# Kernel tuning notes

Measured on AMD Instinct MI355X. Metric: run time of the kernel, lower is better.

Reference implementation:

```python
import jax, jax.numpy as jnp
import numpy as np

N = 20000
E = 320000
IN_DIM = 256
HID = 128
OUT = 64
HEADS = [4, 1]
NEG_SLOPE = 0.2


def setup_inputs() -> dict:
    key = jax.random.key(0)
    ks = jax.random.split(key, 12)
    x = jax.random.normal(ks[0], (N, IN_DIM), dtype=jnp.float32)
    src = jax.random.randint(ks[1], (E,), 0, N, dtype=jnp.int32)
    dst = jax.random.randint(ks[2], (E,), 0, N, dtype=jnp.int32)
    # Layer 0: in=256 -> heads=4, feat=128
    H0, D0 = HEADS[0], HID
    W1 = jax.random.normal(ks[3], (IN_DIM, H0 * D0), dtype=jnp.float32) * (1.0 / np.sqrt(IN_DIM))
    al1 = jax.random.normal(ks[4], (H0, D0), dtype=jnp.float32) * 0.1
    ar1 = jax.random.normal(ks[5], (H0, D0), dtype=jnp.float32) * 0.1
    b1 = jnp.zeros((H0 * D0,), dtype=jnp.float32)
    # Layer 1: in=4*128=512 -> heads=1, feat=64
    IN2 = H0 * D0
    H1, D1 = HEADS[1], OUT
    W2 = jax.random.normal(ks[6], (IN2, H1 * D1), dtype=jnp.float32) * (1.0 / np.sqrt(IN2))
    al2 = jax.random.normal(ks[7], (H1, D1), dtype=jnp.float32) * 0.1
    ar2 = jax.random.normal(ks[8], (H1, D1), dtype=jnp.float32) * 0.1
    b2 = jnp.zeros((H1 * D1,), dtype=jnp.float32)
    return {"x": x, "src": src, "dst": dst, "W1": W1, "al1": al1, "ar1": ar1, "b1": b1,
            "W2": W2, "al2": al2, "ar2": ar2, "b2": b2}


def gat_conv(h, src, dst, W, al, ar, b, num_heads, out_feats):
    # h: [N, F_in]; DGL GATConv, eval mode (no dropout), allow_zero_in_degree.
    feat = (h @ W).reshape(-1, num_heads, out_feats)          # [N,H,D]
    el = jnp.sum(feat * al, axis=-1)                          # [N,H]
    er = jnp.sum(feat * ar, axis=-1)                          # [N,H]
    e = jax.nn.leaky_relu(el[src] + er[dst], NEG_SLOPE)       # [E,H]
    # edge softmax over incoming edges of each dst node (numerically stable)
    m = jax.ops.segment_max(e, dst, num_segments=N)           # [N,H] (-inf for 0-in-degree)
    ex = jnp.exp(e - m[dst])                                  # [E,H]
    s = jax.ops.segment_sum(ex, dst, num_segments=N)          # [N,H]
    alpha = ex / s[dst]                                       # [E,H]
    msg = feat[src] * alpha[:, :, None]                       # [E,H,D]
    rst = jax.ops.segment_sum(msg, dst, num_segments=N)       # [N,H,D]
    return rst + b.reshape(1, num_heads, out_feats)


def reference(x, src, dst, W1, al1, ar1, b1, W2, al2, ar2, b2):
    h = gat_conv(x, src, dst, W1, al1, ar1, b1, HEADS[0], HID)   # [N,4,128]
    h = jax.nn.elu(h)                                            # activation on non-last layer
    h = h.reshape(N, HEADS[0] * HID)                             # flatten(1)
    h = gat_conv(h, src, dst, W2, al2, ar2, b2, HEADS[1], OUT)   # [N,1,64]
    return h.mean(axis=1)                                        # [N,64]
```

## Files before the change

kernel.cpp:

```cpp
#include <hip/hip_runtime.h>
#include <hip/hip_bf16.h>
#include <cstdint>
#include <cstddef>

#define N_NODES 20000
#define N_EDGES 320000
#define IN_DIM  256
#define HID     128
#define OUT_DIM 64
#define H0      4
#define CAP     64

static __device__ __forceinline__ float leaky(float x) { return x > 0.f ? x : 0.2f * x; }

using short8  = __attribute__((ext_vector_type(8))) short;
using short4v = __attribute__((ext_vector_type(4))) short;
using f32x4   = __attribute__((ext_vector_type(4))) float;

struct HL { short h; short l; };
static __device__ __forceinline__ HL split_bf16(float x) {
  HL r;
  __hip_bfloat16 hb = __float2bfloat16(x);
  float hf = __bfloat162float(hb);
  __hip_bfloat16 lb = __float2bfloat16(x - hf);
  r.h = *(short*)&hb;
  r.l = *(short*)&lb;
  return r;
}

static __device__ __forceinline__ short f2bf_bits(float x) {
  __hip_bfloat16 hb = __float2bfloat16(x);
  return *(short*)&hb;
}

static __device__ __forceinline__ float bf16bits_to_f32(short b) {
  uint32_t u = ((uint32_t)(uint16_t)b) << 16;
  return __uint_as_float(u);
}

static __device__ __forceinline__ void fma8(float a, short8 f, float* acc) {
  const uint32_t* d = (const uint32_t*)&f;
#pragma unroll
  for (int q = 0; q < 4; q++) {
    uint32_t u = d[q];
    float lo = __uint_as_float(u << 16);
    float hi = __uint_as_float(u & 0xFFFF0000u);
    acc[2 * q]     += a * lo;
    acc[2 * q + 1] += a * hi;
  }
}

__global__ void presplit_all_kernel(const float* __restrict__ x,
                                    const float* __restrict__ W1,
                                    const float* __restrict__ W2,
                                    short* __restrict__ xh,
                                    short* __restrict__ w1h, short* __restrict__ w1l,
                                    short* __restrict__ w2h, short* __restrict__ w2l,
                                    int* __restrict__ fill) {
  const int X4  = N_NODES * IN_DIM / 4;
  const int NW1 = IN_DIM * (H0 * HID);
  const int NW2 = (H0 * HID) * OUT_DIM;
  int i = blockIdx.x * 256 + threadIdx.x;
  if (i < X4) {
    int base = i * 4;
    float4 v = *(const float4*)&x[base];
    short4v hv;
    hv[0] = f2bf_bits(v.x); hv[1] = f2bf_bits(v.y);
    hv[2] = f2bf_bits(v.z); hv[3] = f2bf_bits(v.w);
    *(short4v*)&xh[base] = hv;
    return;
  }
  int j = i - X4;
  if (j < NW1) {
    int nn = j / IN_DIM, kk = j - nn * IN_DIM;
    HL e = split_bf16(W1[(size_t)kk * (H0 * HID) + nn]);
    w1h[j] = e.h; w1l[j] = e.l;
    return;
  }
  int k = j - NW1;
  if (k < NW2) {
    int nn = k / (H0 * HID), kk = k - nn * (H0 * HID);
    HL e = split_bf16(W2[(size_t)kk * OUT_DIM + nn]);
    w2h[k] = e.h; w2l[k] = e.l;
    return;
  }
  int z = k - NW2;
  if (z < N_NODES) fill[z] = 0;
}

#define LDK 40

template <int BM, int BN, int NH>
static __device__ void gemm_body(int h, int row0,
                                 const short* __restrict__ A,
                                 const short* __restrict__ Bth,
                                 const short* __restrict__ Btl,
                                 float* __restrict__ C,
                                 __hip_bfloat16* __restrict__ Cb,
                                 const float* __restrict__ alv,
                                 const float* __restrict__ arv,
                                 float* __restrict__ el,
                                 float* __restrict__ er,
                                 int M, int K) {
  constexpr int MI = BM / 32;
  constexpr int NT = BN / 32;
  constexpr int NOUT = NH * BN;
  constexpr int TPRA = 256 / BM, KPTA = 32 / TPRA;
  constexpr int TPRB = 256 / BN, KPTB = 32 / TPRB;
  __shared__ short Ash[BM * LDK];
  __shared__ short Bsh[BN * LDK];
  __shared__ short Bsl[BN * LDK];
  __shared__ float els[2][BM], ers[2][BM];
  const int tid  = threadIdx.x;
  const int lane = tid & 63;
  const int wave = tid >> 6;
  const int wm = (wave >> 1) * (BM / 2);
  const int wn = (wave & 1) * (BN / 2);
  const int lr = lane & 15;
  const int lq = lane >> 4;
  const int ra = tid / TPRA, ka = (tid % TPRA) * KPTA;
  const int rb = tid / TPRB, kb = (tid % TPRB) * KPTB;

  f32x4 acc[MI][NT];
#pragma unroll
  for (int i = 0; i < MI; i++)
#pragma unroll
    for (int j = 0; j < NT; j++) acc[i][j] = (f32x4){0.f, 0.f, 0.f, 0.f};

  for (int k0 = 0; k0 < K; k0 += 32) {
    {
      const bool ok = (row0 + ra) < M;
      const size_t g = (size_t)(row0 + ra) * K + k0 + ka;
#pragma unroll
      for (int i = 0; i < KPTA / 8; i++) {
        short8 hv = ok ? *(const short8*)&A[g + 8 * i] : (short8){0,0,0,0,0,0,0,0};
        *(short8*)&Ash[ra * LDK + ka + 8 * i] = hv;
      }
    }
    {
      const size_t g = (size_t)(h * BN + rb) * K + k0 + kb;
#pragma unroll
      for (int i = 0; i < KPTB / 8; i++) {
        short8 hv = *(const short8*)&Bth[g + 8 * i];
        short8 lv = *(const short8*)&Btl[g + 8 * i];
        *(short8*)&Bsh[rb * LDK + kb + 8 * i] = hv;
        *(short8*)&Bsl[rb * LDK + kb + 8 * i] = lv;
      }
    }
    __syncthreads();
    short8 a_v[MI], b_h[NT], b_l[NT];
#pragma unroll
    for (int mi = 0; mi < MI; mi++) {
      int r = wm + mi * 16 + lr;
      a_v[mi] = *(const short8*)&Ash[r * LDK + lq * 8];
    }
#pragma unroll
    for (int nj = 0; nj < NT; nj++) {
      int c = wn + nj * 16 + lr;
      b_h[nj] = *(const short8*)&Bsh[c * LDK + lq * 8];
      b_l[nj] = *(const short8*)&Bsl[c * LDK + lq * 8];
    }
#pragma unroll
    for (int mi = 0; mi < MI; mi++) {
#pragma unroll
      for (int nj = 0; nj < NT; nj++) {
        acc[mi][nj] = __builtin_amdgcn_mfma_f32_16x16x32_bf16(a_v[mi], b_l[nj], acc[mi][nj], 0, 0, 0);
        acc[mi][nj] = __builtin_amdgcn_mfma_f32_16x16x32_bf16(a_v[mi], b_h[nj], acc[mi][nj], 0, 0, 0);
      }
    }
    __syncthreads();
  }
  float av[NT], rv[NT];
#pragma unroll
  for (int nj = 0; nj < NT; nj++) {
    int c = h * BN + wn + nj * 16 + lr;
    av[nj] = alv[c];
    rv[nj] = arv[c];
  }
#pragma unroll
  for (int mi = 0; mi < MI; mi++) {
    float pel[4], per[4];
#pragma unroll
    for (int r = 0; r < 4; r++) {
      float se = 0.f, sr2 = 0.f;
#pragma unroll
      for (int nj = 0; nj < NT; nj++) {
        float v = acc[mi][nj][r];
        se  += v * av[nj];
        sr2 += v * rv[nj];
      }
      pel[r] = se; per[r] = sr2;
    }
#pragma unroll
    for (int off = 1; off < 16; off <<= 1) {
#pragma unroll
      for (int r = 0; r < 4; r++) {
        pel[r] += __shfl_xor(pel[r], off);
        per[r] += __shfl_xor(per[r], off);
      }
    }
    int rowb = wm + mi * 16 + lq * 4;
    if (lr == 0) {
#pragma unroll
      for (int r = 0; r < 4; r++) {
        els[wave & 1][rowb + r] = pel[r];
        ers[wave & 1][rowb + r] = per[r];
      }
    }
    int row = row0 + rowb;
#pragma unroll
    for (int r = 0; r < 4; r++) {
      if (row + r < M) {
#pragma unroll
        for (int nj = 0; nj < NT; nj++) {
          float val = acc[mi][nj][r];
          size_t idx = (size_t)(row + r) * NOUT + h * BN + wn + nj * 16 + lr;
          if (C)  C[idx] = val;
          if (Cb) Cb[idx] = __float2bfloat16(val);
        }
      }
    }
  }
  __syncthreads();
  if (tid < BM && row0 + tid < M) {
    el[(size_t)(row0 + tid) * NH + h] = els[0][tid] + els[1][tid];
    er[(size_t)(row0 + tid) * NH + h] = ers[0][tid] + ers[1][tid];
  }
}

#define GEMM0_BLOCKS (H0 * ((N_NODES + 127) / 128))
#define FILL_BLOCKS  ((N_EDGES + 255) / 256)

__global__ __launch_bounds__(256) void fill_gemm0_kernel(
    const int* __restrict__ src, const int* __restrict__ dst,
    int* __restrict__ fill, int* __restrict__ csr_src,
    const short* __restrict__ xh,
    const short* __restrict__ w1h, const short* __restrict__ w1l,
    __hip_bfloat16* __restrict__ feat1b,
    const float* __restrict__ al1, const float* __restrict__ ar1,
    float* __restrict__ el1, float* __restrict__ er1) {
  if (blockIdx.x < GEMM0_BLOCKS) {
    int h = blockIdx.x & 3;
    int row0 = (blockIdx.x >> 2) * 128;
    gemm_body<128, 128, 4>(h, row0, xh, w1h, w1l, (float*)nullptr, feat1b,
                           al1, ar1, el1, er1, N_NODES, IN_DIM);
    return;
  }
  int e = (blockIdx.x - GEMM0_BLOCKS) * 256 + threadIdx.x;
  if (e < N_EDGES) {
    int d = dst[e];
    int p = atomicAdd(&fill[d], 1);
    if (p < CAP) csr_src[d * CAP + p] = src[e];
  }
}

__global__ __launch_bounds__(256) void gemm1_kernel(
    const short* __restrict__ h1b,
    const short* __restrict__ w2h, const short* __restrict__ w2l,
    float* __restrict__ feat2,
    const float* __restrict__ al2, const float* __restrict__ ar2,
    float* __restrict__ el2, float* __restrict__ er2) {
  gemm_body<64, 64, 1>(0, blockIdx.x * 64, h1b, w2h, w2l, feat2,
                       (__hip_bfloat16*)nullptr, al2, ar2, el2, er2,
                       N_NODES, H0 * HID);
}

__global__ __launch_bounds__(256, 8) void agg0_kernel(const int* __restrict__ fillc,
                                                      const int* __restrict__ csr_src,
                                                      const float* __restrict__ el,
                                                      const float* __restrict__ er,
                                                      const __hip_bfloat16* __restrict__ featb,
                                                      const float* __restrict__ bias,
                                                      short* __restrict__ h1b) {
  __shared__ float alpha_s[4][64][4];
  __shared__ int   src_s[4][64];
  int w = threadIdx.x >> 6;
  int n = blockIdx.x * 4 + w;
  int lane = threadIdx.x & 63;
  if (n >= N_NODES) return;
  int deg = min(fillc[n], CAP);
  int start = n * CAP;
  int h = lane >> 4;
  const int dofs = lane * 8;
  float acc[8] = {};
  float4 er4 = *(const float4*)&er[n * 4];

  float4 ev = make_float4(-1e30f, -1e30f, -1e30f, -1e30f);
  int sv = 0;
  if (lane < deg) {
    sv = csr_src[start + lane];
    float4 l4 = *(const float4*)&el[sv * 4];
    ev.x = leaky(l4.x + er4.x); ev.y = leaky(l4.y + er4.y);
    ev.z = leaky(l4.z + er4.z); ev.w = leaky(l4.w + er4.w);
  }
  float4 m = ev;
#pragma unroll
  for (int off = 32; off; off >>= 1) {
    m.x = fmaxf(m.x, __shfl_xor(m.x, off));
    m.y = fmaxf(m.y, __shfl_xor(m.y, off));
    m.z = fmaxf(m.z, __shfl_xor(m.z, off));
    m.w = fmaxf(m.w, __shfl_xor(m.w, off));
  }
  float4 ex = make_float4(0.f, 0.f, 0.f, 0.f);
  if (lane < deg) {
    ex.x = __expf(ev.x - m.x); ex.y = __expf(ev.y - m.y);
    ex.z = __expf(ev.z - m.z); ex.w = __expf(ev.w - m.w);
  }
  float4 ss = ex;
#pragma unroll
  for (int off = 32; off; off >>= 1) {
    ss.x += __shfl_xor(ss.x, off);
    ss.y += __shfl_xor(ss.y, off);
    ss.z += __shfl_xor(ss.z, off);
    ss.w += __shfl_xor(ss.w, off);
  }
  if (lane < deg) {
    float4 a4 = make_float4(ex.x / ss.x, ex.y / ss.y, ex.z / ss.z, ex.w / ss.w);
    *(float4*)&alpha_s[w][lane][0] = a4;
    src_s[w][lane] = sv;
  }

  const short* fb = (const short*)featb;
  int nb = deg & ~3;
  int i = 0;
  for (; i < nb; i += 4) {
    float a0 = alpha_s[w][i + 0][h];
    float a1 = alpha_s[w][i + 1][h];
    float a2 = alpha_s[w][i + 2][h];
    float a3 = alpha_s[w][i + 3][h];
    int s0 = src_s[w][i + 0];
    int s1 = src_s[w][i + 1];
    int s2 = src_s[w][i + 2];
    int s3 = src_s[w][i + 3];
    short8 f0 = *(const short8*)&fb[(size_t)s0 * (H0 * HID) + dofs];
    short8 f1 = *(const short8*)&fb[(size_t)s1 * (H0 * HID) + dofs];
    short8 f2 = *(const short8*)&fb[(size_t)s2 * (H0 * HID) + dofs];
    short8 f3 = *(const short8*)&fb[(size_t)s3 * (H0 * HID) + dofs];
    fma8(a0, f0, acc);
    fma8(a1, f1, acc);
    fma8(a2, f2, acc);
    fma8(a3, f3, acc);
  }
  for (; i < deg; i++) {
    float a = alpha_s[w][i][h];
    int s = src_s[w][i];
    short8 f = *(const short8*)&fb[(size_t)s * (H0 * HID) + dofs];
    fma8(a, f, acc);
  }

  short8 ob;
#pragma unroll
  for (int j = 0; j < 8; j++) {
    float o = acc[j] + bias[dofs + j];
    o = o > 0.f ? o : (__expf(o) - 1.f);
    ob[j] = f2bf_bits(o);
  }
  *(short8*)&h1b[(size_t)n * (H0 * HID) + dofs] = ob;
}

__global__ __launch_bounds__(256) void agg1_kernel(const int* __restrict__ fillc,
                                                   const int* __restrict__ csr_src,
                                                   const float* __restrict__ el,
                                                   const float* __restrict__ er,
                                                   const float* __restrict__ feat,
                                                   const float* __restrict__ bias,
                                                   float* __restrict__ out) {
  __shared__ float alpha_s[4][64];
  __shared__ int   src_s[4][64];
  int w = threadIdx.x >> 6;
  int n = blockIdx.x * 4 + w;
  int lane = threadIdx.x & 63;
  if (n >= N_NODES) return;
  int deg = min(fillc[n], CAP);
  int start = n * CAP;
  float erd = er[n];
  int g = lane >> 4, q = lane & 15;
  float4 acc = make_float4(0.f, 0.f, 0.f, 0.f);

  float ev = -1e30f; int sv = 0;
  if (lane < deg) { sv = csr_src[start + lane]; ev = leaky(el[sv] + erd); }
  float m = ev;
#pragma unroll
  for (int off = 32; off; off >>= 1) m = fmaxf(m, __shfl_xor(m, off));
  float ex = (lane < deg) ? __expf(ev - m) : 0.f;
  float ss = ex;
#pragma unroll
  for (int off = 32; off; off >>= 1) ss += __shfl_xor(ss, off);
  if (lane < deg) { alpha_s[w][lane] = ex / ss; src_s[w][lane] = sv; }

  if (deg > 0) {
    int nit = (deg + 3) >> 2;
    float a_c = 0.f;
    float4 f_c = make_float4(0.f, 0.f, 0.f, 0.f);
    {
      int e = g;
      if (e < deg) {
        a_c = alpha_s[w][e];
        int s = src_s[w][e];
        f_c = *(const float4*)&feat[(size_t)s * OUT_DIM + q * 4];
      }
    }
    for (int it = 1; it < nit; it++) {
      float a_n = 0.f;
      float4 f_n = make_float4(0.f, 0.f, 0.f, 0.f);
      int e = (it << 2) + g;
      if (e < deg) {
        a_n = alpha_s[w][e];
        int s = src_s[w][e];
        f_n = *(const float4*)&feat[(size_t)s * OUT_DIM + q * 4];
      }
      acc.x += a_c * f_c.x; acc.y += a_c * f_c.y;
      acc.z += a_c * f_c.z; acc.w += a_c * f_c.w;
      a_c = a_n; f_c = f_n;
    }
    acc.x += a_c * f_c.x; acc.y += a_c * f_c.y;
    acc.z += a_c * f_c.z; acc.w += a_c * f_c.w;
  }

#pragma unroll
  for (int off = 16; off < 64; off <<= 1) {
    acc.x += __shfl_xor(acc.x, off);
    acc.y += __shfl_xor(acc.y, off);
    acc.z += __shfl_xor(acc.z, off);
    acc.w += __shfl_xor(acc.w, off);
  }
  if (g == 0) {
    float4 b4 = *(const float4*)&bias[q * 4];
    float4 o = make_float4(acc.x + b4.x, acc.y + b4.y, acc.z + b4.z, acc.w + b4.w);
    *(float4*)&out[(size_t)n * OUT_DIM + q * 4] = o;
  }
}

extern "C" void kernel_launch(void* const* d_in, const int* in_sizes, int n_in,
                              void* d_out, int out_size, void* d_ws, size_t ws_size,
                              hipStream_t stream) {
  const float* x   = (const float*)d_in[0];
  const int*   src = (const int*)d_in[1];
  const int*   dst = (const int*)d_in[2];
  const float* W1  = (const float*)d_in[3];
  const float* al1 = (const float*)d_in[4];
  const float* ar1 = (const float*)d_in[5];
  const float* b1  = (const float*)d_in[6];
  const float* W2  = (const float*)d_in[7];
  const float* al2 = (const float*)d_in[8];
  const float* ar2 = (const float*)d_in[9];
  const float* b2  = (const float*)d_in[10];

  char* ws = (char*)d_ws;
  size_t off = 0;
  auto alloc = [&](size_t bytes) -> void* {
    void* p = ws + off;
    off += (bytes + 255) & ~(size_t)255;
    return p;
  };
  int* fill     = (int*)alloc((size_t)N_NODES * 4);
  int* csr_src  = (int*)alloc((size_t)N_NODES * CAP * 4);
  short* xh     = (short*)alloc((size_t)N_NODES * IN_DIM * 2);
  short* W1th   = (short*)alloc((size_t)IN_DIM * (H0 * HID) * 2);
  short* W1tl   = (short*)alloc((size_t)IN_DIM * (H0 * HID) * 2);
  short* W2th   = (short*)alloc((size_t)(H0 * HID) * OUT_DIM * 2);
  short* W2tl   = (short*)alloc((size_t)(H0 * HID) * OUT_DIM * 2);
  __hip_bfloat16* feat1b = (__hip_bfloat16*)alloc((size_t)N_NODES * (H0 * HID) * 2);
  float* el1    = (float*)alloc((size_t)N_NODES * H0 * 4);
  float* er1    = (float*)alloc((size_t)N_NODES * H0 * 4);
  short* h1b    = (short*)alloc((size_t)N_NODES * (H0 * HID) * 2);
  float* feat2  = (float*)alloc((size_t)N_NODES * OUT_DIM * 4);
  float* el2    = (float*)alloc((size_t)N_NODES * 4);
  float* er2    = (float*)alloc((size_t)N_NODES * 4);
  (void)ws_size; (void)in_sizes; (void)n_in; (void)out_size;

  {
    const int total = N_NODES * IN_DIM / 4 + IN_DIM * (H0 * HID) + (H0 * HID) * OUT_DIM
                    + N_NODES;
    presplit_all_kernel<<<(total + 255) / 256, 256, 0, stream>>>(
        x, W1, W2, xh, W1th, W1tl, W2th, W2tl, fill);
  }

  fill_gemm0_kernel<<<GEMM0_BLOCKS + FILL_BLOCKS, 256, 0, stream>>>(
      src, dst, fill, csr_src, xh, W1th, W1tl, feat1b, al1, ar1, el1, er1);

  agg0_kernel<<<(N_NODES + 3) / 4, 256, 0, stream>>>(fill, csr_src, el1, er1, feat1b, b1, h1b);

  gemm1_kernel<<<(N_NODES + 63) / 64, 256, 0, stream>>>(h1b, W2th, W2tl, feat2, al2, ar2, el2, er2);

  agg1_kernel<<<(N_NODES + 3) / 4, 256, 0, stream>>>(fill, csr_src, el2, er2, feat2, b2, (float*)d_out);
}
```

Measured before the change: 195.6 us.

## Split layer-0 aggregation into coefficient kernel and feature-sliced gather kernel

Layer-0 attention aggregation is split in two. A new kernel computes the softmax coefficients per edge and writes them to a global alpha buffer. A second kernel launches eight blocks per node group, each handling one 64-column feature slice. Each wave processes eight edges in parallel with a software-prefetched gather, then reduces the partial sums by shuffle. This aims to raise parallelism and memory-level concurrency in the gather, at the cost of an extra launch, a global alpha round-trip, and redundant CSR and alpha loads across slices.

```diff
diff --git a/kernel.cpp b/kernel.cpp
--- a/kernel.cpp
+++ b/kernel.cpp
@@ -265,24 +265,17 @@
                        N_NODES, H0 * HID);
 }
 
-__global__ __launch_bounds__(256, 8) void agg0_kernel(const int* __restrict__ fillc,
-                                                      const int* __restrict__ csr_src,
-                                                      const float* __restrict__ el,
-                                                      const float* __restrict__ er,
-                                                      const __hip_bfloat16* __restrict__ featb,
-                                                      const float* __restrict__ bias,
-                                                      short* __restrict__ h1b) {
-  __shared__ float alpha_s[4][64][4];
-  __shared__ int   src_s[4][64];
+__global__ __launch_bounds__(256) void coef0_kernel(const int* __restrict__ fillc,
+                                                    const int* __restrict__ csr_src,
+                                                    const float* __restrict__ el,
+                                                    const float* __restrict__ er,
+                                                    float* __restrict__ alpha4) {
   int w = threadIdx.x >> 6;
   int n = blockIdx.x * 4 + w;
   int lane = threadIdx.x & 63;
   if (n >= N_NODES) return;
   int deg = min(fillc[n], CAP);
   int start = n * CAP;
-  int h = lane >> 4;
-  const int dofs = lane * 8;
-  float acc[8] = {};
   float4 er4 = *(const float4*)&er[n * 4];
 
   float4 ev = make_float4(-1e30f, -1e30f, -1e30f, -1e30f);
@@ -316,46 +309,74 @@
   }
   if (lane < deg) {
     float4 a4 = make_float4(ex.x / ss.x, ex.y / ss.y, ex.z / ss.z, ex.w / ss.w);
-    *(float4*)&alpha_s[w][lane][0] = a4;
-    src_s[w][lane] = sv;
+    *(float4*)&alpha4[(size_t)(start + lane) * 4] = a4;
+  }
+}
+
+__global__ __launch_bounds__(256) void agg0s_kernel(const int* __restrict__ fillc,
+                                                    const int* __restrict__ csr_src,
+                                                    const float* __restrict__ alpha4,
+                                                    const __hip_bfloat16* __restrict__ featb,
+                                                    const float* __restrict__ bias,
+                                                    short* __restrict__ h1b) {
+  int s  = blockIdx.x & 7;
+  int nb = blockIdx.x >> 3;
+  int w = threadIdx.x >> 6;
+  int n = nb * 4 + w;
+  int lane = threadIdx.x & 63;
+  if (n >= N_NODES) return;
+  int g = lane >> 3, q = lane & 7;
+  int deg = min(fillc[n], CAP);
+  int start = n * CAP;
+  int h = s >> 1;
+
+  __shared__ float a_s[4][64];
+  __shared__ int   s_s[4][64];
+  if (lane < deg) {
+    s_s[w][lane] = csr_src[start + lane];
+    a_s[w][lane] = alpha4[(size_t)(start + lane) * 4 + h];
   }
 
   const short* fb = (const short*)featb;
-  int nb = deg & ~3;
-  int i = 0;
-  for (; i < nb; i += 4) {
-    float a0 = alpha_s[w][i + 0][h];
-    float a1 = alpha_s[w][i + 1][h];
-    float a2 = alpha_s[w][i + 2][h];
-    float a3 = alpha_s[w][i + 3][h];
-    int s0 = src_s[w][i + 0];
-    int s1 = src_s[w][i + 1];
-    int s2 = src_s[w][i + 2];
-    int s3 = src_s[w][i + 3];
-    short8 f0 = *(const short8*)&fb[(size_t)s0 * (H0 * HID) + dofs];
-    short8 f1 = *(const short8*)&fb[(size_t)s1 * (H0 * HID) + dofs];
-    short8 f2 = *(const short8*)&fb[(size_t)s2 * (H0 * HID) + dofs];
-    short8 f3 = *(const short8*)&fb[(size_t)s3 * (H0 * HID) + dofs];
-    fma8(a0, f0, acc);
-    fma8(a1, f1, acc);
-    fma8(a2, f2, acc);
-    fma8(a3, f3, acc);
-  }
-  for (; i < deg; i++) {
-    float a = alpha_s[w][i][h];
-    int s = src_s[w][i];
-    short8 f = *(const short8*)&fb[(size_t)s * (H0 * HID) + dofs];
-    fma8(a, f, acc);
-  }
-
-  short8 ob;
-#pragma unroll
-  for (int j = 0; j < 8; j++) {
-    float o = acc[j] + bias[dofs + j];
-    o = o > 0.f ? o : (__expf(o) - 1.f);
-    ob[j] = f2bf_bits(o);
-  }
-  *(short8*)&h1b[(size_t)n * (H0 * HID) + dofs] = ob;
+  const int fofs = s * 64 + q * 8;
+  float acc[8] = {};
+  if (deg > 0) {
+    int nit = (deg + 7) >> 3;
+    float a_c = 0.f;
+    short8 f_c = (short8){0, 0, 0, 0, 0, 0, 0, 0};
+    int e0 = g;
+    if (e0 < deg) {
+      a_c = a_s[w][e0];
+      f_c = *(const short8*)&fb[(size_t)s_s[w][e0] * (H0 * HID) + fofs];
+    }
+    for (int it = 1; it < nit; it++) {
+      float a_n = 0.f;
+      short8 f_n = (short8){0, 0, 0, 0, 0, 0, 0, 0};
+      int e = (it << 3) + g;
+      if (e < deg) {
+        a_n = a_s[w][e];
+        f_n = *(const short8*)&fb[(size_t)s_s[w][e] * (H0 * HID) + fofs];
+      }
+      fma8(a_c, f_c, acc);
+      a_c = a_n; f_c = f_n;
+    }
+    fma8(a_c, f_c, acc);
+  }
+#pragma unroll
+  for (int off = 8; off < 64; off <<= 1) {
+#pragma unroll
+    for (int j = 0; j < 8; j++) acc[j] += __shfl_xor(acc[j], off);
+  }
+  if (g == 0) {
+    short8 ob;
+#pragma unroll
+    for (int j = 0; j < 8; j++) {
+      float o = acc[j] + bias[s * 64 + q * 8 + j];
+      o = o > 0.f ? o : (__expf(o) - 1.f);
+      ob[j] = f2bf_bits(o);
+    }
+    *(short8*)&h1b[(size_t)n * (H0 * HID) + s * 64 + q * 8] = ob;
+  }
 }
 
 __global__ __launch_bounds__(256) void agg1_kernel(const int* __restrict__ fillc,
@@ -463,6 +484,7 @@
   __hip_bfloat16* feat1b = (__hip_bfloat16*)alloc((size_t)N_NODES * (H0 * HID) * 2);
   float* el1    = (float*)alloc((size_t)N_NODES * H0 * 4);
   float* er1    = (float*)alloc((size_t)N_NODES * H0 * 4);
+  float* alpha4 = (float*)alloc((size_t)N_NODES * CAP * 4 * 4);
   short* h1b    = (short*)alloc((size_t)N_NODES * (H0 * HID) * 2);
   float* feat2  = (float*)alloc((size_t)N_NODES * OUT_DIM * 4);
   float* el2    = (float*)alloc((size_t)N_NODES * 4);
@@ -479,7 +501,10 @@
   fill_gemm0_kernel<<<GEMM0_BLOCKS + FILL_BLOCKS, 256, 0, stream>>>(
       src, dst, fill, csr_src, xh, W1th, W1tl, feat1b, al1, ar1, el1, er1);
 
-  agg0_kernel<<<(N_NODES + 3) / 4, 256, 0, stream>>>(fill, csr_src, el1, er1, feat1b, b1, h1b);
+  coef0_kernel<<<(N_NODES + 3) / 4, 256, 0, stream>>>(fill, csr_src, el1, er1, alpha4);
+
+  agg0s_kernel<<<((N_NODES + 3) / 4) * 8, 256, 0, stream>>>(
+      fill, csr_src, alpha4, feat1b, b1, h1b);
 
   gemm1_kernel<<<(N_NODES + 63) / 64, 256, 0, stream>>>(h1b, W2th, W2tl, feat2, al2, ar2, el2, er2);
 
```

New measurement: 215.1 us. +9.9%, slower.

## Split layer-0 aggregation into coefficient kernel and column-sliced gather kernel

Applied to the files above, without the earlier changes.

The fused agg0 kernel is split in two. A coef0 kernel computes per-edge softmax coefficients and writes them head-major to a global buffer. An agg0s kernel then has each block handle 32 nodes for a single 64-column slice of the 512-wide feature, with 8 threads per node and the 8 slices spread across consecutive blocks. The aim is to narrow each block's gather footprint for better cache locality and more parallelism, at the cost of an extra launch and an extra global round-trip for the alpha buffer.

```diff
diff --git a/kernel.cpp b/kernel.cpp
--- a/kernel.cpp
+++ b/kernel.cpp
@@ -265,24 +265,17 @@
                        N_NODES, H0 * HID);
 }
 
-__global__ __launch_bounds__(256, 8) void agg0_kernel(const int* __restrict__ fillc,
-                                                      const int* __restrict__ csr_src,
-                                                      const float* __restrict__ el,
-                                                      const float* __restrict__ er,
-                                                      const __hip_bfloat16* __restrict__ featb,
-                                                      const float* __restrict__ bias,
-                                                      short* __restrict__ h1b) {
-  __shared__ float alpha_s[4][64][4];
-  __shared__ int   src_s[4][64];
+__global__ __launch_bounds__(256) void coef0_kernel(const int* __restrict__ fillc,
+                                                    const int* __restrict__ csr_src,
+                                                    const float* __restrict__ el,
+                                                    const float* __restrict__ er,
+                                                    float* __restrict__ alphaT) {
   int w = threadIdx.x >> 6;
   int n = blockIdx.x * 4 + w;
   int lane = threadIdx.x & 63;
   if (n >= N_NODES) return;
   int deg = min(fillc[n], CAP);
   int start = n * CAP;
-  int h = lane >> 4;
-  const int dofs = lane * 8;
-  float acc[8] = {};
   float4 er4 = *(const float4*)&er[n * 4];
 
   float4 ev = make_float4(-1e30f, -1e30f, -1e30f, -1e30f);
@@ -315,47 +308,62 @@
     ss.w += __shfl_xor(ss.w, off);
   }
   if (lane < deg) {
-    float4 a4 = make_float4(ex.x / ss.x, ex.y / ss.y, ex.z / ss.z, ex.w / ss.w);
-    *(float4*)&alpha_s[w][lane][0] = a4;
-    src_s[w][lane] = sv;
-  }
+    const int NC = N_NODES * CAP;
+    int p = start + lane;
+    alphaT[0 * NC + p] = ex.x / ss.x;
+    alphaT[1 * NC + p] = ex.y / ss.y;
+    alphaT[2 * NC + p] = ex.z / ss.z;
+    alphaT[3 * NC + p] = ex.w / ss.w;
+  }
+}
+
+__global__ __launch_bounds__(256) void agg0s_kernel(const int* __restrict__ fillc,
+                                                    const int* __restrict__ csr_src,
+                                                    const float* __restrict__ alphaT,
+                                                    const __hip_bfloat16* __restrict__ featb,
+                                                    const float* __restrict__ bias,
+                                                    short* __restrict__ h1b) {
+  int s  = blockIdx.x & 7;
+  int nb = blockIdx.x >> 3;
+  int tid = threadIdx.x;
+  int j = tid >> 3;
+  int q = tid & 7;
+  int n = nb * 32 + j;
+  int h = s >> 1;
+
+  __shared__ int2 as_s[32][CAP];
+
+  int deg = 0;
+  if (n < N_NODES) deg = min(fillc[n], CAP);
+  int start = n * CAP;
+  const int NC = N_NODES * CAP;
+  for (int slot = q; slot < deg; slot += 8) {
+    int2 v;
+    v.x = csr_src[start + slot];
+    v.y = __float_as_int(alphaT[h * NC + start + slot]);
+    as_s[j][slot] = v;
+  }
+  __syncthreads();
 
   const short* fb = (const short*)featb;
-  int nb = deg & ~3;
-  int i = 0;
-  for (; i < nb; i += 4) {
-    float a0 = alpha_s[w][i + 0][h];
-    float a1 = alpha_s[w][i + 1][h];
-    float a2 = alpha_s[w][i + 2][h];
-    float a3 = alpha_s[w][i + 3][h];
-    int s0 = src_s[w][i + 0];
-    int s1 = src_s[w][i + 1];
-    int s2 = src_s[w][i + 2];
-    int s3 = src_s[w][i + 3];
-    short8 f0 = *(const short8*)&fb[(size_t)s0 * (H0 * HID) + dofs];
-    short8 f1 = *(const short8*)&fb[(size_t)s1 * (H0 * HID) + dofs];
-    short8 f2 = *(const short8*)&fb[(size_t)s2 * (H0 * HID) + dofs];
-    short8 f3 = *(const short8*)&fb[(size_t)s3 * (H0 * HID) + dofs];
-    fma8(a0, f0, acc);
-    fma8(a1, f1, acc);
-    fma8(a2, f2, acc);
-    fma8(a3, f3, acc);
-  }
-  for (; i < deg; i++) {
-    float a = alpha_s[w][i][h];
-    int s = src_s[w][i];
-    short8 f = *(const short8*)&fb[(size_t)s * (H0 * HID) + dofs];
-    fma8(a, f, acc);
-  }
-
-  short8 ob;
-#pragma unroll
-  for (int j = 0; j < 8; j++) {
-    float o = acc[j] + bias[dofs + j];
-    o = o > 0.f ? o : (__expf(o) - 1.f);
-    ob[j] = f2bf_bits(o);
-  }
-  *(short8*)&h1b[(size_t)n * (H0 * HID) + dofs] = ob;
+  const int fofs = s * 64 + q * 8;
+  float acc[8] = {};
+  for (int i = 0; i < deg; i++) {
+    int2 v = as_s[j][i];
+    short8 f = *(const short8*)&fb[(v.x << 9) + fofs];
+    fma8(__int_as_float(v.y), f, acc);
+  }
+
+  if (n < N_NODES) {
+    short8 ob;
+#pragma unroll
+    for (int jj = 0; jj < 8; jj++) {
+      float o = acc[jj] + bias[fofs + jj];
+      o = o > 0.f ? o : (__expf(o) - 1.f);
+      ob[jj] = f2bf_bits(o);
+    }
+    *(short8*)&h1b[((size_t)n << 9) + fofs] = ob;
+  }
 }
 
 __global__ __launch_bounds__(256) void agg1_kernel(const int* __restrict__ fillc,
@@ -463,6 +471,7 @@
   __hip_bfloat16* feat1b = (__hip_bfloat16*)alloc((size_t)N_NODES * (H0 * HID) * 2);
   float* el1    = (float*)alloc((size_t)N_NODES * H0 * 4);
   float* er1    = (float*)alloc((size_t)N_NODES * H0 * 4);
+  float* alphaT = (float*)alloc((size_t)H0 * N_NODES * CAP * 4);
   short* h1b    = (short*)alloc((size_t)N_NODES * (H0 * HID) * 2);
   float* feat2  = (float*)alloc((size_t)N_NODES * OUT_DIM * 4);
   float* el2    = (float*)alloc((size_t)N_NODES * 4);
@@ -479,7 +488,10 @@
   fill_gemm0_kernel<<<GEMM0_BLOCKS + FILL_BLOCKS, 256, 0, stream>>>(
       src, dst, fill, csr_src, xh, W1th, W1tl, feat1b, al1, ar1, el1, er1);
 
-  agg0_kernel<<<(N_NODES + 3) / 4, 256, 0, stream>>>(fill, csr_src, el1, er1, feat1b, b1, h1b);
+  coef0_kernel<<<(N_NODES + 3) / 4, 256, 0, stream>>>(fill, csr_src, el1, er1, alphaT);
+
+  agg0s_kernel<<<((N_NODES + 31) / 32) * 8, 256, 0, stream>>>(
+      fill, csr_src, alphaT, feat1b, b1, h1b);
 
   gemm1_kernel<<<(N_NODES + 63) / 64, 256, 0, stream>>>(h1b, W2th, W2tl, feat2, al2, ar2, el2, er2);
 
```

After: 185.7 us. -5.1%, faster.
